# Kernel optimization log

Measured on AMD Instinct MI355X. Metric: run time of the kernel, lower is better.

The kernel has to match this reference:

```python
import jax, jax.numpy as jnp
import numpy as np

TOPK = 10
HID = 512
RHID = 150
CH = 32


def _gru(x, Wi, Wh, bi, bh):
    """torch nn.GRU (1 layer, batch_first) with gate order r,z,n. x: [B,T,D]."""
    H = Wh.shape[1]
    xi = x @ Wi.T + bi  # [B,T,3H] precompute input projections

    def step(h, xt):
        gh = h @ Wh.T + bh
        r = jax.nn.sigmoid(xt[:, :H] + gh[:, :H])
        z = jax.nn.sigmoid(xt[:, H:2 * H] + gh[:, H:2 * H])
        n = jnp.tanh(xt[:, 2 * H:] + r * gh[:, 2 * H:])
        h_new = (1.0 - z) * n + z * h
        return h_new, h_new

    h0 = jnp.zeros((x.shape[0], H), x.dtype)
    hT, ys = jax.lax.scan(step, h0, jnp.swapaxes(xi, 0, 1))
    return jnp.swapaxes(ys, 0, 1), hT


def reference(window, emb, w_init, w_root, arma_b, Wi1, Wh1, bi1, bh1,
              Wi2, Wh2, bi2, bh2, W_fc, b_fc):
    B, T, N = window.shape
    # --- SingleEmbedding (post-warmup): cosine similarity + per-row top-k ---
    Wn = emb / jnp.clip(jnp.linalg.norm(emb, axis=1, keepdims=True), 1e-8, None)
    A = Wn @ Wn.T
    A = A * (1.0 - jnp.eye(N, dtype=A.dtype))  # fill_diagonal_(0)
    A = jnp.maximum(A, 0.0)                    # clamp(0)
    vals, idx = jax.lax.top_k(A, TOPK)         # [N, TOPK]
    # zero-valued edges kept with weight 0: identical math (zero degree/message contribution)
    src = jnp.repeat(jnp.arange(N), TOPK)      # edge source = row i
    dst = idx.reshape(-1)                      # edge dest = col j
    attr = vals.reshape(-1)
    # --- batch edges over B (offset b*N), then over T (offset t*B*N), as in torch code ---
    boff = jnp.arange(B) * N
    bsrc = (src[None, :] + boff[:, None]).reshape(-1)   # [B*E]
    bdst = (dst[None, :] + boff[:, None]).reshape(-1)
    battr = jnp.tile(attr, B)
    toff = jnp.arange(T) * (B * N)
    fsrc = (bsrc[None, :] + toff[:, None]).reshape(-1)  # [T*B*E]
    fdst = (bdst[None, :] + toff[:, None]).reshape(-1)
    fattr = jnp.tile(battr, T)
    Ntot = B * N * T
    # node layout (b, n, t): flat row = (b*N + n)*T + t  (faithful to torch view order)
    x = jnp.transpose(window, (0, 2, 1)).reshape(Ntot, 1)
    # --- ARMAConv: 1 stack, 1 layer, GELU, gcn_norm without self-loops ---
    deg = jax.ops.segment_sum(fattr, fdst, num_segments=Ntot)
    dinv = jnp.where(deg > 0, jax.lax.rsqrt(jnp.where(deg > 0, deg, 1.0)), 0.0)
    enorm = dinv[fsrc] * fattr * dinv[fdst]
    h = x @ w_init                                            # [Ntot, CH]
    agg = jax.ops.segment_sum(h[fsrc] * enorm[:, None], fdst, num_segments=Ntot)
    out = jax.nn.gelu(agg + x @ w_root + arma_b, approximate=False)
    # --- add node embedding, GRU encode ---
    xt = out.reshape(B, N, T, CH).transpose(0, 2, 1, 3) + emb  # [B,T,N,CH]
    xt = xt.reshape(B, T, N * CH)
    _, h_end = _gru(xt, Wi1, Wh1, bi1, bh1)                   # [B, HID]
    # --- ReconstructionModel: repeat_interleave(T, dim=1).view(B,T,-1) then GRU+fc ---
    hrep = jnp.repeat(h_end, T, axis=1).reshape(B, T, HID)
    dec, _ = _gru(hrep, Wi2, Wh2, bi2, bh2)                   # [B,T,RHID]
    return dec @ W_fc.T + b_fc


def setup_inputs():
    key = jax.random.key(0)
    ks = jax.random.split(key, 10)
    B, T, N = 32, 100, 150
    d_in = N * CH
    return {
        "window": jax.random.normal(ks[0], (B, T, N), jnp.float32),
        "emb": jax.random.normal(ks[1], (N, CH), jnp.float32) * 0.3,
        "w_init": jax.random.normal(ks[2], (1, CH), jnp.float32) * 0.5,
        "w_root": jax.random.normal(ks[3], (1, CH), jnp.float32) * 0.5,
        "arma_b": jnp.zeros((CH,), jnp.float32),
        "Wi1": jax.random.normal(ks[4], (3 * HID, d_in), jnp.float32) * (1.0 / np.sqrt(d_in)),
        "Wh1": jax.random.normal(ks[5], (3 * HID, HID), jnp.float32) * (1.0 / np.sqrt(HID)),
        "bi1": jnp.zeros((3 * HID,), jnp.float32),
        "bh1": jnp.zeros((3 * HID,), jnp.float32),
        "Wi2": jax.random.normal(ks[6], (3 * RHID, HID), jnp.float32) * (1.0 / np.sqrt(HID)),
        "Wh2": jax.random.normal(ks[7], (3 * RHID, RHID), jnp.float32) * (1.0 / np.sqrt(RHID)),
        "bi2": jnp.zeros((3 * RHID,), jnp.float32),
        "bh2": jnp.zeros((3 * RHID,), jnp.float32),
        "W_fc": jax.random.normal(ks[8], (N, RHID), jnp.float32) * (1.0 / np.sqrt(RHID)),
        "b_fc": jnp.zeros((N,), jnp.float32),
    }
```

## Files before the change

kernel.cpp:

```cpp
#include <hip/hip_runtime.h>
#include <hip/hip_fp16.h>
#include <math.h>

typedef _Float16 f16;
typedef _Float16 half8 __attribute__((ext_vector_type(8)));
typedef _Float16 half4 __attribute__((ext_vector_type(4)));
typedef float float4v __attribute__((ext_vector_type(4)));
typedef float float2v __attribute__((ext_vector_type(2)));
typedef unsigned int uint4v __attribute__((ext_vector_type(4)));

#define AS1 __attribute__((address_space(1)))
#define AS3 __attribute__((address_space(3)))

constexpr size_t alup(size_t x){ return (x + 255) & ~(size_t)255; }
constexpr size_t OFF_MT   = 0;
constexpr size_t OFF_DEG  = alup(OFF_MT + 150*150*4);
constexpr size_t OFF_HT0  = alup(OFF_DEG + 150*4);
constexpr size_t OFF_HT1  = alup(OFF_HT0 + (size_t)32*512*4);
constexpr size_t OFF_WFCP = alup(OFF_HT1 + (size_t)32*512*4);
constexpr size_t OFF_WH2P = alup(OFF_WFCP + (size_t)256*192*2);
constexpr size_t OFF_DECB = alup(OFF_WH2P + (size_t)512*160*2);
constexpr size_t ZONE_END = alup(OFF_DECB + (size_t)3200*192*2);
constexpr size_t OFF_EDST = ZONE_END;
constexpr size_t OFF_EVAL = alup(OFF_EDST + 1500*4);
constexpr size_t OFF_PT   = alup(OFF_EVAL + 1500*4);
constexpr size_t OFF_XF   = alup(OFF_PT + (size_t)513*452*4);
constexpr size_t OFF_SS   = alup(OFF_XF + (size_t)480000*4);
constexpr size_t OFF_XT   = alup(OFF_SS + (size_t)480000*4);
constexpr size_t OFF_WI1H = alup(OFF_XT + (size_t)3200*4800*2);
constexpr size_t OFF_XI1  = alup(OFF_WI1H + (size_t)1536*4800*2);
constexpr size_t OFF_XI2  = alup(OFF_XI1 + (size_t)3200*1536*2);

static __device__ __forceinline__ float fsig(float x){ return 1.0f/(1.0f + __expf(-x)); }
static __device__ __forceinline__ float ftanh(float x){
    x = fminf(fmaxf(x, -15.f), 15.f);
    float e = __expf(2.0f*x);
    return (e - 1.0f)/(e + 1.0f);
}

__global__ void k_topk(const float* __restrict__ emb, int* __restrict__ EDST,
                       float* __restrict__ EVAL, float* __restrict__ DEG) {
    __shared__ float WnT[32*152];
    __shared__ float invn[160];
    __shared__ float As[160];
    int tid = threadIdx.x;
    int i = blockIdx.x;
    for (int idx = tid; idx < 4800; idx += 256) {
        int jj = idx >> 5, c = idx & 31;
        WnT[c*152 + jj] = emb[idx];
    }
    __syncthreads();
    if (tid < 150) {
        float s = 0.f;
        #pragma unroll
        for (int c = 0; c < 32; ++c) { float v = WnT[c*152 + tid]; s += v*v; }
        invn[tid] = 1.0f / fmaxf(sqrtf(s), 1e-8f);
    }
    __syncthreads();
    for (int idx = tid; idx < 4800; idx += 256) {
        int jj = idx >> 5, c = idx & 31;
        WnT[c*152 + jj] *= invn[jj];
    }
    __syncthreads();
    int j = tid;
    if (j < 150) {
        float a = 0.f;
        #pragma unroll
        for (int c = 0; c < 32; ++c) a += WnT[c*152 + i] * WnT[c*152 + j];
        a = (j == i) ? 0.f : fmaxf(a, 0.f);
        As[j] = a;
    }
    __syncthreads();
    if (j < 150) {
        float aj = As[j];
        int cnt = 0;
        for (int m = 0; m < 150; ++m) {
            float am = As[m];
            cnt += (am > aj) || (am == aj && m < j);
        }
        if (cnt < 10) {
            EDST[i*10 + cnt] = j;
            EVAL[i*10 + cnt] = aj;
            atomicAdd(&DEG[j], aj);
        }
    }
}

__global__ void k_prep(const int* __restrict__ EDST, const float* __restrict__ EVAL,
                       const float* __restrict__ DEG, float* __restrict__ MT,
                       const float* __restrict__ Wi1, f16* __restrict__ WI1H,
                       const float* __restrict__ W_fc, f16* __restrict__ WFCP,
                       const float* __restrict__ Wh2, f16* __restrict__ WH2P,
                       const float* __restrict__ window, float* __restrict__ XF,
                       const float* __restrict__ Wi2, float* __restrict__ PT) {
    int b = blockIdx.x, tid = threadIdx.x;
    if (b == 0) {
        __shared__ float dinv[160];
        if (tid < 150) {
            float d = DEG[tid];
            dinv[tid] = (d > 0.f) ? rsqrtf(d) : 0.f;
        }
        __syncthreads();
        for (int e = tid; e < 1500; e += 256) {
            int src = e / 10;
            int dst = EDST[e];
            MT[src*150 + dst] = dinv[src] * EVAL[e] * dinv[dst];
        }
    } else if (b < 28801) {
        int idx = (b - 1)*256 + tid;
        WI1H[idx] = (f16)Wi1[idx];
    } else if (b < 28889) {
        int idx = (b - 28801)*256 + tid;
        if (idx < 22500) {
            int r = idx / 150, c = idx % 150;
            WFCP[r*192 + c] = (f16)W_fc[idx];
        }
    } else if (b < 29153) {
        int idx = (b - 28889)*256 + tid;
        if (idx < 67500) {
            int r = idx / 150, c = idx % 150;
            WH2P[r*160 + c] = (f16)Wh2[idx];
        }
    } else if (b < 31028) {
        int idx = (b - 29153)*256 + tid;
        float v = window[idx];
        int bb = idx / 15000;
        int r = idx % 15000;
        int t = r / 150, n = r % 150;
        XF[bb*15000 + n*100 + t] = v;
    } else {
        int o = (b - 31028)*256 + tid;
        if (o < 450) {
            float run = 0.f;
            PT[o] = 0.f;
            for (int k = 0; k < 512; ++k) {
                run += Wi2[o*512 + k];
                PT[(size_t)(k+1)*452 + o] = run;
            }
        }
    }
}

__global__ void k_conv(const float* __restrict__ XF, const float* __restrict__ MT,
                       float* __restrict__ SS) {
    __shared__ float xs[152];
    int tid = threadIdx.x;
    int base = blockIdx.x * 150;
    if (tid < 150) xs[tid] = XF[base + tid];
    __syncthreads();
    if (tid < 150) {
        float s = 0.f;
        for (int m = 0; m < 150; ++m) s += MT[m*150 + tid] * xs[m];
        SS[base + tid] = s;
    }
}

__global__ void k_xt(const float* __restrict__ SS, const float* __restrict__ XF,
                     const float* __restrict__ w_init, const float* __restrict__ w_root,
                     const float* __restrict__ arma_b, const float* __restrict__ emb,
                     f16* __restrict__ xt) {
    __shared__ float ssl[152];
    __shared__ float xfl[152];
    int tid = threadIdx.x;
    int bid = blockIdx.x;
    int b = bid / 100, t = bid % 100;
    if (tid < 150) {
        int f = b*15000 + tid*100 + t;
        ssl[tid] = SS[f];
        xfl[tid] = XF[f];
    }
    __syncthreads();
    for (int e = tid; e < 4800; e += 256) {
        int n = e >> 5, c = e & 31;
        float pre = ssl[n]*w_init[c] + xfl[n]*w_root[c] + arma_b[c];
        float g = 0.5f * pre * (1.0f + erff(pre * 0.70710678118654752f));
        xt[(size_t)bid*4800 + e] = (f16)(g + emb[e]);
    }
}

template <typename TC>
__global__ void k_gemm(const f16* __restrict__ A, const f16* __restrict__ Bm,
                       const float* __restrict__ bias, TC* __restrict__ C,
                       int K, int ldc, int nvalid, int ntm) {
    __shared__ f16 As[64*64];
    __shared__ f16 Bs[128*64];
    int tid = threadIdx.x;
    int lane = tid & 63, wave = tid >> 6;
    int wm = wave >> 1, wn = wave & 1;
    int tm = blockIdx.x % ntm, tn = blockIdx.x / ntm;
    int m0 = tm * 64, n0 = tn * 128;
    int lrow = lane & 15, quad = lane >> 4;

    float4v acc[2][4];
    #pragma unroll
    for (int mi = 0; mi < 2; ++mi)
        #pragma unroll
        for (int ni = 0; ni < 4; ++ni)
            acc[mi][ni] = (float4v){0.f, 0.f, 0.f, 0.f};

    for (int k0 = 0; k0 < K; k0 += 64) {
        #pragma unroll
        for (int i = 0; i < 2; ++i) {
            int cid = i*256 + tid;
            int row = cid >> 3, cq = cid & 7;
            int cbase = cid & ~63;
            const f16* ga = A + (size_t)(m0+row)*K + k0 + cq*8;
            __builtin_amdgcn_global_load_lds((const AS1 void*)ga, (AS3 void*)(As + cbase*8), 16, 0, 0);
        }
        #pragma unroll
        for (int i = 0; i < 4; ++i) {
            int cid = i*256 + tid;
            int row = cid >> 3, cq = cid & 7;
            int cbase = cid & ~63;
            const f16* gb = Bm + (size_t)(n0+row)*K + k0 + cq*8;
            __builtin_amdgcn_global_load_lds((const AS1 void*)gb, (AS3 void*)(Bs + cbase*8), 16, 0, 0);
        }
        __syncthreads();
        #pragma unroll
        for (int kk = 0; kk < 2; ++kk) {
            half8 aF[2], bF[4];
            #pragma unroll
            for (int mi = 0; mi < 2; ++mi)
                aF[mi] = *(const half8*)&As[(wm*32 + mi*16 + lrow)*64 + kk*32 + quad*8];
            #pragma unroll
            for (int ni = 0; ni < 4; ++ni)
                bF[ni] = *(const half8*)&Bs[(wn*64 + ni*16 + lrow)*64 + kk*32 + quad*8];
            #pragma unroll
            for (int mi = 0; mi < 2; ++mi)
                #pragma unroll
                for (int ni = 0; ni < 4; ++ni)
                    acc[mi][ni] = __builtin_amdgcn_mfma_f32_16x16x32_f16(aF[mi], bF[ni], acc[mi][ni], 0, 0, 0);
        }
        __syncthreads();
    }

    #pragma unroll
    for (int ni = 0; ni < 4; ++ni) {
        int gcol = n0 + wn*64 + ni*16 + lrow;
        if (gcol >= nvalid) continue;
        float bv = bias[gcol];
        #pragma unroll
        for (int mi = 0; mi < 2; ++mi) {
            int growb = m0 + wm*32 + mi*16 + quad*4;
            #pragma unroll
            for (int r = 0; r < 4; ++r)
                C[(size_t)(growb + r)*ldc + gcol] = (TC)(acc[mi][ni][r] + bv);
        }
    }
}

__global__ __launch_bounds__(256, 1)
void k_gru1(const f16* __restrict__ xi1, const float* __restrict__ Wh1,
            const float* __restrict__ bh1, unsigned* __restrict__ ht0,
            unsigned* __restrict__ ht1) {
    __shared__ __align__(16) f16 hA[16*640];
    __shared__ float ghs[192];
    int tid = threadIdx.x;
    int g = blockIdx.x & 15;
    int j = blockIdx.x >> 4;
    int b0 = g * 2;
    int lane = tid & 63, wave = tid >> 6;
    int lrow = lane & 15, quad = lane >> 4;

    half8 Bf0[16], Bf1[16];
    if (wave < 3) {
        #pragma unroll
        for (int tile = 0; tile < 2; ++tile) {
            int rr = (wave*2 + tile)*16 + lrow;
            int grow = (rr >> 5)*512 + (j << 5) + (rr & 31);
            const float* wp = Wh1 + (size_t)grow*512 + quad*8;
            #pragma unroll
            for (int k0 = 0; k0 < 16; ++k0) {
                float4v w0 = *(const float4v*)(wp + k0*32);
                float4v w1 = *(const float4v*)(wp + k0*32 + 4);
                half8 hb;
                hb[0]=(f16)w0[0]; hb[1]=(f16)w0[1]; hb[2]=(f16)w0[2]; hb[3]=(f16)w0[3];
                hb[4]=(f16)w1[0]; hb[5]=(f16)w1[1]; hb[6]=(f16)w1[2]; hb[7]=(f16)w1[3];
                if (tile == 0) Bf0[k0] = hb; else Bf1[k0] = hb;
            }
        }
    }

    float hold = 0.f, bhr = 0.f, bhz = 0.f, bhn = 0.f;
    f16 xir = (f16)0.f, xiz = (f16)0.f, xin = (f16)0.f;
    size_t xb = 0;
    if (tid < 64) {
        int bl = tid >> 5, i = tid & 31;
        int col = (j << 5) + i;
        bhr = bh1[col]; bhz = bh1[512 + col]; bhn = bh1[1024 + col];
        xb = (size_t)((b0 + bl)*100)*1536 + col;
        xir = xi1[xb]; xiz = xi1[xb + 512]; xin = xi1[xb + 1024];
    }
    int sbl = tid >> 7;
    int kb  = (tid & 127) << 2;

    for (int t = 0; t < 100; ++t) {
        const unsigned* cur = (t & 1) ? ht1 : ht0;
        unsigned* nxt = (t & 1) ? ht0 : ht1;
        {
            const unsigned* p = cur + (size_t)(b0 + sbl)*512 + kb;
            uint4v A4;
            unsigned tagw = (unsigned)t << 16;
            for (;;) {
                asm volatile("global_load_dwordx4 %0, %1, off sc0 sc1\n\ts_waitcnt vmcnt(0)"
                             : "=v"(A4) : "v"(p) : "memory");
                if ((A4[0] & 0xffff0000u) == tagw && (A4[1] & 0xffff0000u) == tagw &&
                    (A4[2] & 0xffff0000u) == tagw && (A4[3] & 0xffff0000u) == tagw) break;
                __builtin_amdgcn_s_sleep(1);
            }
            union { unsigned short s[4]; half4 h; } cv;
            cv.s[0] = (unsigned short)A4[0]; cv.s[1] = (unsigned short)A4[1];
            cv.s[2] = (unsigned short)A4[2]; cv.s[3] = (unsigned short)A4[3];
            *(half4*)&hA[(kb >> 5)*640 + sbl*40 + (kb & 31)] = cv.h;
        }
        __syncthreads();

        if (wave < 3) {
            float4v a0a = (float4v){0.f,0.f,0.f,0.f}, a0b = a0a, a1a = a0a, a1b = a0a;
            const f16* aB = &hA[lrow*40 + quad*8];
            #pragma unroll
            for (int k0 = 0; k0 < 16; k0 += 2) {
                half8 a0 = *(const half8*)(aB + k0*640);
                half8 a1 = *(const half8*)(aB + (k0+1)*640);
                a0a = __builtin_amdgcn_mfma_f32_16x16x32_f16(a0, Bf0[k0], a0a, 0, 0, 0);
                a1a = __builtin_amdgcn_mfma_f32_16x16x32_f16(a0, Bf1[k0], a1a, 0, 0, 0);
                a0b = __builtin_amdgcn_mfma_f32_16x16x32_f16(a1, Bf0[k0+1], a0b, 0, 0, 0);
                a1b = __builtin_amdgcn_mfma_f32_16x16x32_f16(a1, Bf1[k0+1], a1b, 0, 0, 0);
            }
            if (lane < 16) {
                int n0 = wave*2, n1 = n0 + 1;
                ghs[n0*16 + lane]      = a0a[0] + a0b[0];
                ghs[96 + n0*16 + lane] = a0a[1] + a0b[1];
                ghs[n1*16 + lane]      = a1a[0] + a1b[0];
                ghs[96 + n1*16 + lane] = a1a[1] + a1b[1];
            }
        }
        __syncthreads();

        if (tid < 64) {
            int bl = tid >> 5, i = tid & 31;
            float xr_ = (float)xir, xz_ = (float)xiz, xn_ = (float)xin;
            int tn = (t < 99) ? t + 1 : 99;
            size_t xo = xb + (size_t)tn*1536;
            xir = xi1[xo]; xiz = xi1[xo + 512]; xin = xi1[xo + 1024];
            float gr = ghs[bl*96 + i]      + bhr;
            float gz = ghs[bl*96 + 32 + i] + bhz;
            float gn = ghs[bl*96 + 64 + i] + bhn;
            float r = fsig(xr_ + gr);
            float z = fsig(xz_ + gz);
            float n = ftanh(xn_ + r*gn);
            float hnew = (1.f - z)*n + z*hold;
            hold = hnew;
            union { f16 h; unsigned short s; } hb; hb.h = (f16)hnew;
            unsigned pk = ((unsigned)(t + 1) << 16) | (unsigned)hb.s;
            __hip_atomic_store(nxt + (size_t)(b0 + bl)*512 + (j << 5) + i, pk,
                               __ATOMIC_RELAXED, __HIP_MEMORY_SCOPE_AGENT);
        }
    }
}

__global__ void k_xi2(const unsigned* __restrict__ ht0, const float* __restrict__ PT,
                      const float* __restrict__ bi2, f16* __restrict__ xi2) {
    __shared__ float hs[512];
    int tid = threadIdx.x;
    int bid = blockIdx.x;
    int b = bid / 100, t = bid % 100;
    {
        union { unsigned short s; f16 h; } c1, c2;
        c1.s = (unsigned short)ht0[(b << 9) + tid];
        c2.s = (unsigned short)ht0[(b << 9) + tid + 256];
        hs[tid] = (float)c1.h;
        hs[tid + 256] = (float)c2.h;
    }
    __syncthreads();
    int base = t * 512;
    int m0 = base / 100;
    #pragma unroll
    for (int q = 0; q < 2; ++q) {
        int o = tid + q*256;
        if (o < 450) {
            float acc = bi2[o];
            #pragma unroll
            for (int s = 0; s < 7; ++s) {
                int klo = (m0 + s)*100 - base;     klo = klo < 0 ? 0 : klo;
                int khi = (m0 + s + 1)*100 - base; khi = khi > 512 ? 512 : khi;
                if (klo < khi) {
                    float seg = PT[(size_t)khi*452 + o] - PT[(size_t)klo*452 + o];
                    acc += hs[m0 + s] * seg;
                }
            }
            xi2[(size_t)bid*512 + o] = (f16)acc;
        }
    }
}

__global__ __launch_bounds__(256, 1)
void k_gru2(const f16* __restrict__ xi2, const f16* __restrict__ wh2p,
            const float* __restrict__ bh2, f16* __restrict__ decb) {
    __shared__ __align__(16) f16 hA[5*640];
    __shared__ float ghs[512];
    int tid = threadIdx.x;
    int b = blockIdx.x;
    int lane = tid & 63, wave = tid >> 6;
    int lrow = lane & 15, quad = lane >> 4;

    for (int i = tid; i < 5*640; i += 256) hA[i] = (f16)0.f;

    half8 Bf[8][5];
    #pragma unroll
    for (int tt = 0; tt < 8; ++tt) {
        int rn = (wave*8 + tt)*16 + lrow;
        const f16* wp = wh2p + (size_t)rn*160 + quad*8;
        #pragma unroll
        for (int k0 = 0; k0 < 5; ++k0)
            Bf[tt][k0] = *(const half8*)(wp + k0*32);
    }

    float hold = 0.f, bhr = 0.f, bhz = 0.f, bhn = 0.f;
    f16 xr = (f16)0.f, xz = (f16)0.f, xn = (f16)0.f;
    size_t xbase = (size_t)b * 100 * 512;
    if (tid < 150) {
        bhr = bh2[tid]; bhz = bh2[150 + tid]; bhn = bh2[300 + tid];
        xr = xi2[xbase + tid]; xz = xi2[xbase + 150 + tid]; xn = xi2[xbase + 300 + tid];
    }
    __syncthreads();

    for (int t = 0; t < 100; ++t) {
        float4v acc[8];
        #pragma unroll
        for (int tt = 0; tt < 8; ++tt) acc[tt] = (float4v){0.f,0.f,0.f,0.f};
        #pragma unroll
        for (int k0 = 0; k0 < 5; ++k0) {
            half8 a = *(const half8*)&hA[k0*640 + lrow*40 + quad*8];
            #pragma unroll
            for (int tt = 0; tt < 8; ++tt)
                acc[tt] = __builtin_amdgcn_mfma_f32_16x16x32_f16(a, Bf[tt][k0], acc[tt], 0, 0, 0);
        }
        if (lane < 16) {
            #pragma unroll
            for (int tt = 0; tt < 8; ++tt)
                ghs[(wave*8 + tt)*16 + lane] = acc[tt][0];
        }
        __syncthreads();

        if (tid < 150) {
            float r = fsig((float)xr + ghs[tid] + bhr);
            float z = fsig((float)xz + ghs[150 + tid] + bhz);
            float n = ftanh((float)xn + r*(ghs[300 + tid] + bhn));
            float hnew = (1.f - z)*n + z*hold;
            hold = hnew;
            f16 hh = (f16)hnew;
            hA[(tid >> 5)*640 + (tid & 31)] = hh;
            decb[((size_t)b*100 + t)*192 + tid] = hh;
            int tn = (t < 99) ? t + 1 : 99;
            size_t xo = xbase + (size_t)tn*512;
            xr = xi2[xo + tid]; xz = xi2[xo + 150 + tid]; xn = xi2[xo + 300 + tid];
        }
        __syncthreads();
    }
}

extern "C" void kernel_launch(void* const* d_in, const int* in_sizes, int n_in,
                              void* d_out, int out_size, void* d_ws, size_t ws_size,
                              hipStream_t stream) {
    const float* window = (const float*)d_in[0];
    const float* emb    = (const float*)d_in[1];
    const float* w_init = (const float*)d_in[2];
    const float* w_root = (const float*)d_in[3];
    const float* arma_b = (const float*)d_in[4];
    const float* Wi1    = (const float*)d_in[5];
    const float* Wh1    = (const float*)d_in[6];
    const float* bi1    = (const float*)d_in[7];
    const float* bh1    = (const float*)d_in[8];
    const float* Wi2    = (const float*)d_in[9];
    const float* Wh2    = (const float*)d_in[10];
    const float* bi2    = (const float*)d_in[11];
    const float* bh2    = (const float*)d_in[12];
    const float* W_fc   = (const float*)d_in[13];
    const float* b_fc   = (const float*)d_in[14];
    float* out = (float*)d_out;

    char* ws = (char*)d_ws;
    float*    MT   = (float*)(ws + OFF_MT);
    float*    DEG  = (float*)(ws + OFF_DEG);
    unsigned* HT0  = (unsigned*)(ws + OFF_HT0);
    unsigned* HT1  = (unsigned*)(ws + OFF_HT1);
    f16*      WFCP = (f16*)  (ws + OFF_WFCP);
    f16*      WH2P = (f16*)  (ws + OFF_WH2P);
    f16*      DECB = (f16*)  (ws + OFF_DECB);
    int*      EDST = (int*)  (ws + OFF_EDST);
    float*    EVAL = (float*)(ws + OFF_EVAL);
    float*    PT   = (float*)(ws + OFF_PT);
    float*    XF   = (float*)(ws + OFF_XF);
    float*    SS   = (float*)(ws + OFF_SS);
    f16*      XT   = (f16*)  (ws + OFF_XT);
    f16*      WI1H = (f16*)  (ws + OFF_WI1H);
    f16*      XI1H = (f16*)  (ws + OFF_XI1);
    f16*      XI2H = (f16*)  (ws + OFF_XI2);

    hipMemsetAsync(d_ws, 0, ZONE_END, stream);

    k_topk<<<150, 256, 0, stream>>>(emb, EDST, EVAL, DEG);

    k_prep<<<31030, 256, 0, stream>>>(EDST, EVAL, DEG, MT,
                                      Wi1, WI1H, W_fc, WFCP, Wh2, WH2P,
                                      window, XF, Wi2, PT);

    k_conv<<<3200, 256, 0, stream>>>(XF, MT, SS);
    k_xt<<<3200, 256, 0, stream>>>(SS, XF, w_init, w_root, arma_b, emb, XT);

    k_gemm<f16><<<50*12, 256, 0, stream>>>(XT, WI1H, bi1, XI1H, 4800, 1536, 1536, 50);

    k_gru1<<<256, 256, 0, stream>>>(XI1H, Wh1, bh1, HT0, HT1);

    k_xi2<<<3200, 256, 0, stream>>>(HT0, PT, bi2, XI2H);

    k_gru2<<<32, 256, 0, stream>>>(XI2H, WH2P, bh2, DECB);

    k_gemm<float><<<50*2, 256, 0, stream>>>(DECB, WFCP, b_fc, out, 192, 150, 150, 50);

    (void)in_sizes; (void)n_in; (void)out_size; (void)ws_size;
}
```

Baseline: 541.0 us.

## Fuse GRU2 input projection into recurrent kernel and parallelize prefix-sum prep

Removes the separate k_xi2 launch and its xi2 global buffer. Each GRU2 block now computes the next timestep's input projection from prefix sums while the MFMA recurrence runs, double-buffering it in shared memory. The Wi2 prefix-sum prep becomes a wave-level shuffle scan, one row per wave, instead of a serial 512-step loop per thread. This saves a launch and a global round trip, but adds projection work inside the latency-bound 32-block recurrent loop.

```diff
diff --git a/kernel.cpp b/kernel.cpp
--- a/kernel.cpp
+++ b/kernel.cpp
@@ -6,7 +6,6 @@
 typedef _Float16 half8 __attribute__((ext_vector_type(8)));
 typedef _Float16 half4 __attribute__((ext_vector_type(4)));
 typedef float float4v __attribute__((ext_vector_type(4)));
-typedef float float2v __attribute__((ext_vector_type(2)));
 typedef unsigned int uint4v __attribute__((ext_vector_type(4)));
 
 #define AS1 __attribute__((address_space(1)))
@@ -29,7 +28,6 @@
 constexpr size_t OFF_XT   = alup(OFF_SS + (size_t)480000*4);
 constexpr size_t OFF_WI1H = alup(OFF_XT + (size_t)3200*4800*2);
 constexpr size_t OFF_XI1  = alup(OFF_WI1H + (size_t)1536*4800*2);
-constexpr size_t OFF_XI2  = alup(OFF_XI1 + (size_t)3200*1536*2);
 
 static __device__ __forceinline__ float fsig(float x){ return 1.0f/(1.0f + __expf(-x)); }
 static __device__ __forceinline__ float ftanh(float x){
@@ -129,13 +127,25 @@
         int t = r / 150, n = r % 150;
         XF[bb*15000 + n*100 + t] = v;
     } else {
-        int o = (b - 31028)*256 + tid;
-        if (o < 450) {
-            float run = 0.f;
-            PT[o] = 0.f;
-            for (int k = 0; k < 512; ++k) {
-                run += Wi2[o*512 + k];
-                PT[(size_t)(k+1)*452 + o] = run;
+        int row = (b - 31028)*4 + (tid >> 6);
+        int lane = tid & 63;
+        if (row < 450) {
+            const float* src = Wi2 + (size_t)row*512 + lane*8;
+            float v[8]; float s = 0.f;
+            #pragma unroll
+            for (int i = 0; i < 8; ++i) { v[i] = src[i]; s += v[i]; }
+            float inc = s;
+            #pragma unroll
+            for (int d = 1; d < 64; d <<= 1) {
+                float up = __shfl_up(inc, d, 64);
+                if (lane >= d) inc += up;
+            }
+            float run = inc - s;
+            if (lane == 0) PT[row] = 0.f;
+            #pragma unroll
+            for (int i = 0; i < 8; ++i) {
+                run += v[i];
+                PT[(size_t)(lane*8 + i + 1)*452 + row] = run;
             }
         }
     }
@@ -359,12 +369,19 @@
     }
 }
 
-__global__ void k_xi2(const unsigned* __restrict__ ht0, const float* __restrict__ PT,
-                      const float* __restrict__ bi2, f16* __restrict__ xi2) {
+__global__ __launch_bounds__(256, 1)
+void k_gru2(const unsigned* __restrict__ ht0, const float* __restrict__ PT,
+            const float* __restrict__ bi2, const f16* __restrict__ wh2p,
+            const float* __restrict__ bh2, f16* __restrict__ decb) {
+    __shared__ __align__(16) f16 hA[5*640];
+    __shared__ float ghs[512];
     __shared__ float hs[512];
+    __shared__ float xis[2][456];
     int tid = threadIdx.x;
-    int bid = blockIdx.x;
-    int b = bid / 100, t = bid % 100;
+    int b = blockIdx.x;
+    int lane = tid & 63, wave = tid >> 6;
+    int lrow = lane & 15, quad = lane >> 4;
+
     {
         union { unsigned short s; f16 h; } c1, c2;
         c1.s = (unsigned short)ht0[(b << 9) + tid];
@@ -372,39 +389,8 @@
         hs[tid] = (float)c1.h;
         hs[tid + 256] = (float)c2.h;
     }
-    __syncthreads();
-    int base = t * 512;
-    int m0 = base / 100;
-    #pragma unroll
-    for (int q = 0; q < 2; ++q) {
-        int o = tid + q*256;
-        if (o < 450) {
-            float acc = bi2[o];
-            #pragma unroll
-            for (int s = 0; s < 7; ++s) {
-                int klo = (m0 + s)*100 - base;     klo = klo < 0 ? 0 : klo;
-                int khi = (m0 + s + 1)*100 - base; khi = khi > 512 ? 512 : khi;
-                if (klo < khi) {
-                    float seg = PT[(size_t)khi*452 + o] - PT[(size_t)klo*452 + o];
-                    acc += hs[m0 + s] * seg;
-                }
-            }
-            xi2[(size_t)bid*512 + o] = (f16)acc;
-        }
-    }
-}
-
-__global__ __launch_bounds__(256, 1)
-void k_gru2(const f16* __restrict__ xi2, const f16* __restrict__ wh2p,
-            const float* __restrict__ bh2, f16* __restrict__ decb) {
-    __shared__ __align__(16) f16 hA[5*640];
-    __shared__ float ghs[512];
-    int tid = threadIdx.x;
-    int b = blockIdx.x;
-    int lane = tid & 63, wave = tid >> 6;
-    int lrow = lane & 15, quad = lane >> 4;
-
     for (int i = tid; i < 5*640; i += 256) hA[i] = (f16)0.f;
+    __syncthreads();
 
     half8 Bf[8][5];
     #pragma unroll
@@ -417,11 +403,28 @@
     }
 
     float hold = 0.f, bhr = 0.f, bhz = 0.f, bhn = 0.f;
-    f16 xr = (f16)0.f, xz = (f16)0.f, xn = (f16)0.f;
-    size_t xbase = (size_t)b * 100 * 512;
+    float b2a = bi2[tid < 450 ? tid : 0];
+    float b2b = (tid + 256 < 450) ? bi2[tid + 256] : 0.f;
     if (tid < 150) {
         bhr = bh2[tid]; bhz = bh2[150 + tid]; bhn = bh2[300 + tid];
-        xr = xi2[xbase + tid]; xz = xi2[xbase + 150 + tid]; xn = xi2[xbase + 300 + tid];
+    }
+    {
+        int m0 = 0;
+        #pragma unroll
+        for (int q = 0; q < 2; ++q) {
+            int o = tid + q*256;
+            if (o < 450) {
+                float acc = q ? b2b : b2a;
+                #pragma unroll
+                for (int s = 0; s < 7; ++s) {
+                    int klo = (m0 + s)*100;     klo = klo < 0 ? 0 : klo;
+                    int khi = (m0 + s + 1)*100; khi = khi > 512 ? 512 : khi;
+                    if (klo < khi)
+                        acc += hs[m0 + s] * (PT[(size_t)khi*452 + o] - PT[(size_t)klo*452 + o]);
+                }
+                xis[0][o] = acc;
+            }
+        }
     }
     __syncthreads();
 
@@ -441,20 +444,37 @@
             for (int tt = 0; tt < 8; ++tt)
                 ghs[(wave*8 + tt)*16 + lane] = acc[tt][0];
         }
+        if (t < 99) {
+            int base = (t + 1) * 512;
+            int m0 = base / 100;
+            #pragma unroll
+            for (int q = 0; q < 2; ++q) {
+                int o = tid + q*256;
+                if (o < 450) {
+                    float acc2 = q ? b2b : b2a;
+                    #pragma unroll
+                    for (int s = 0; s < 7; ++s) {
+                        int klo = (m0 + s)*100 - base;     klo = klo < 0 ? 0 : klo;
+                        int khi = (m0 + s + 1)*100 - base; khi = khi > 512 ? 512 : khi;
+                        if (klo < khi)
+                            acc2 += hs[m0 + s] * (PT[(size_t)khi*452 + o] - PT[(size_t)klo*452 + o]);
+                    }
+                    xis[(t + 1) & 1][o] = acc2;
+                }
+            }
+        }
         __syncthreads();
 
         if (tid < 150) {
-            float r = fsig((float)xr + ghs[tid] + bhr);
-            float z = fsig((float)xz + ghs[150 + tid] + bhz);
-            float n = ftanh((float)xn + r*(ghs[300 + tid] + bhn));
+            const float* xc = xis[t & 1];
+            float r = fsig(xc[tid] + ghs[tid] + bhr);
+            float z = fsig(xc[150 + tid] + ghs[150 + tid] + bhz);
+            float n = ftanh(xc[300 + tid] + r*(ghs[300 + tid] + bhn));
             float hnew = (1.f - z)*n + z*hold;
             hold = hnew;
             f16 hh = (f16)hnew;
             hA[(tid >> 5)*640 + (tid & 31)] = hh;
             decb[((size_t)b*100 + t)*192 + tid] = hh;
-            int tn = (t < 99) ? t + 1 : 99;
-            size_t xo = xbase + (size_t)tn*512;
-            xr = xi2[xo + tid]; xz = xi2[xo + 150 + tid]; xn = xi2[xo + 300 + tid];
         }
         __syncthreads();
     }
@@ -496,13 +516,12 @@
     f16*      XT   = (f16*)  (ws + OFF_XT);
     f16*      WI1H = (f16*)  (ws + OFF_WI1H);
     f16*      XI1H = (f16*)  (ws + OFF_XI1);
-    f16*      XI2H = (f16*)  (ws + OFF_XI2);
 
     hipMemsetAsync(d_ws, 0, ZONE_END, stream);
 
     k_topk<<<150, 256, 0, stream>>>(emb, EDST, EVAL, DEG);
 
-    k_prep<<<31030, 256, 0, stream>>>(EDST, EVAL, DEG, MT,
+    k_prep<<<31141, 256, 0, stream>>>(EDST, EVAL, DEG, MT,
                                       Wi1, WI1H, W_fc, WFCP, Wh2, WH2P,
                                       window, XF, Wi2, PT);
 
@@ -513,9 +532,7 @@
 
     k_gru1<<<256, 256, 0, stream>>>(XI1H, Wh1, bh1, HT0, HT1);
 
-    k_xi2<<<3200, 256, 0, stream>>>(HT0, PT, bi2, XI2H);
-
-    k_gru2<<<32, 256, 0, stream>>>(XI2H, WH2P, bh2, DECB);
+    k_gru2<<<32, 256, 0, stream>>>(HT0, PT, bi2, WH2P, bh2, DECB);
 
     k_gemm<float><<<50*2, 256, 0, stream>>>(DECB, WFCP, b_fc, out, 192, 150, 150, 50);
 
```

New measurement: 692.2 us. 1.28x slower.
